# Kernel tuning notes

Hardware: AMD Instinct MI355X
Metric: run time of the kernel (lower is better)

Reference implementation:

```python
import jax, jax.numpy as jnp
import numpy as np

B, T, D, H = 32, 512, 512, 8
DH = D // H  # 64


def _pos_enc(t, d):
    # pos / 10000^(2i/d) for ALL i, then sin on even cols, cos on odd cols, scaled by sqrt(d)
    pos = np.arange(t, dtype=np.float64)[:, None]
    i = np.arange(d, dtype=np.float64)[None, :]
    ang = pos / np.power(10000.0, 2.0 * i / d)
    pe = np.empty((t, d), dtype=np.float64)
    pe[:, 0::2] = np.sin(ang[:, 0::2])
    pe[:, 1::2] = np.cos(ang[:, 1::2])
    return jnp.asarray(pe * np.sqrt(float(d)), dtype=jnp.float32)


def setup_inputs() -> dict:
    key = jax.random.key(0)
    ks = jax.random.split(key, 9)
    return {
        "queries": jax.random.normal(ks[0], (B, T, D), dtype=jnp.float32),
        "keys": jax.random.normal(ks[1], (B, T, D), dtype=jnp.float32),
        "query_masks": jax.random.randint(ks[2], (B,), 0, T, dtype=jnp.int32),
        "key_masks": jax.random.randint(ks[3], (B,), 0, T, dtype=jnp.int32),
        "W_Q": jax.random.normal(ks[4], (D, D), dtype=jnp.float32) * 0.05,
        "W_K": jax.random.normal(ks[5], (D, D), dtype=jnp.float32) * 0.05,
        "W_V": jax.random.normal(ks[6], (D, D), dtype=jnp.float32) * 0.05,
        "fw1": jax.random.normal(ks[7], (D, 4 * D), dtype=jnp.float32) * 0.05,
        "fw2": jax.random.normal(ks[8], (4 * D, D), dtype=jnp.float32) * 0.05,
    }


def reference(queries, keys, query_masks, key_masks, W_Q, W_K, W_V, fw1, fw2):
    pe = _pos_enc(T, D)  # [T, D]
    # Source bug kept: queries = posenc(queries); keys = posenc(queries)  -> keys input unused
    q1 = queries + pe[None]          # [B,T,D]
    k1 = q1 + pe[None]               # pos-encoded twice
    Q = q1 @ W_Q                     # [B,T,D]
    Kp = k1 @ W_K                    # [B,T,D]
    V = Kp @ W_V                     # source bug kept: values from projected keys
    # split heads (head-major fold in the original concat(split) idiom)
    Qh = Q.reshape(B, T, H, DH).transpose(2, 0, 1, 3)   # [H,B,T,dh]
    Kh = Kp.reshape(B, T, H, DH).transpose(2, 0, 1, 3)
    Vh = V.reshape(B, T, H, DH).transpose(2, 0, 1, 3)
    scores = jnp.einsum('hbqd,hbkd->hbqk', Qh, Kh) / jnp.sqrt(jnp.float32(DH))
    # source subtracts max over the QUERY axis (axis=1 of [H*B,T,T]) = axis 2 here
    scores = scores - scores.max(axis=2, keepdims=True)
    attn = jax.nn.softmax(scores, axis=-1)
    qmask = (jnp.arange(T)[None, :] < query_masks[:, None]).astype(jnp.float32)  # [B,T]
    attn = attn * qmask[None, :, :, None]
    out = jnp.einsum('hbqk,hbkd->hbqd', attn, Vh)       # [H,B,T,dh]
    result = out.transpose(1, 2, 0, 3).reshape(B, T, D) + q1  # residual with pos-encoded queries
    hidden = jax.nn.relu(result @ fw1)                  # [B,T,4D]
    result = result + hidden @ fw2                      # residual; no layer norm (use_layer_norm=False)
    return result
```

## Files before the change

kernel.cpp:

```cpp
#include <hip/hip_runtime.h>
#include <cstdint>
#include <cstddef>

typedef __bf16 bf16x8 __attribute__((ext_vector_type(8)));
typedef float f32x4 __attribute__((ext_vector_type(4)));
using u16 = unsigned short;
using u32 = unsigned int;

__device__ __forceinline__ u16 f2b(float f) {
  u32 u = __float_as_uint(f);
  u32 r = u + 0x7FFFu + ((u >> 16) & 1u);
  return (u16)(r >> 16);
}
__device__ __forceinline__ float b2f(u16 h) { return __uint_as_float((u32)h << 16); }

__device__ __forceinline__ void gload16(const void* g, void* l) {
  __builtin_amdgcn_global_load_lds((const __attribute__((address_space(1))) void*)g,
                                   (__attribute__((address_space(3))) void*)l, 16, 0, 0);
}

__device__ __forceinline__ u32 mapf(float f) {
  u32 u = __float_as_uint(f);
  return (u & 0x80000000u) ? ~u : (u | 0x80000000u);
}
__device__ __forceinline__ float unmapf(u32 k) {
  u32 u = (k & 0x80000000u) ? (k ^ 0x80000000u) : ~k;
  return __uint_as_float(u);
}
__device__ __forceinline__ u32 cvtpk(float lo, float hi) {
  u32 r;
  asm("v_cvt_pk_bf16_f32 %0, %1, %2" : "=v"(r) : "v"(lo), "v"(hi));
  return r;
}

#define MFMA __builtin_amdgcn_mfma_f32_16x16x32_bf16

__global__ void pe_kernel(float* __restrict__ pe) {
  int i = blockIdx.x * 256 + threadIdx.x;
  if (i >= 512 * 512) return;
  int t = i >> 9, d = i & 511;
  double ang = (double)t * exp((double)d * (-2.0 / 512.0) * log(10000.0));
  double v = (d & 1) ? cos(ang) : sin(ang);
  pe[i] = (float)(v * 22.627416997969522);
}

__global__ __launch_bounds__(256) void wprep_kernel(
    const float* __restrict__ WQ, const float* __restrict__ WK, const float* __restrict__ WV,
    const float* __restrict__ f1, const float* __restrict__ f2, u16* __restrict__ WQth,
    u16* __restrict__ WQtl, u16* __restrict__ WKth, u16* __restrict__ WKtl,
    u16* __restrict__ WVt, u16* __restrict__ f1t, u16* __restrict__ f2t,
    u16* __restrict__ WKb) {
  __shared__ float tile[64][65];
  const int bid = blockIdx.x, t = threadIdx.x;
  if (bid >= 704) {
    int i4 = (bid - 704) * 256 + t;
    float4 v = *(const float4*)&WK[i4 * 4];
    ushort4 o = {f2b(v.x), f2b(v.y), f2b(v.z), f2b(v.w)};
    *(ushort4*)&WKb[i4 * 4] = o;
    return;
  }
  const float* in;
  int R, C, bx, by;
  u16 *oh, *ol;
  bool split;
  if (bid < 64) {
    in = WQ; R = 512; C = 512; oh = WQth; ol = WQtl; split = true; bx = bid % 8; by = bid / 8;
  } else if (bid < 128) {
    int l = bid - 64;
    in = WK; R = 512; C = 512; oh = WKth; ol = WKtl; split = true; bx = l % 8; by = l / 8;
  } else if (bid < 192) {
    int l = bid - 128;
    in = WV; R = 512; C = 512; oh = WVt; ol = nullptr; split = false; bx = l % 8; by = l / 8;
  } else if (bid < 448) {
    int l = bid - 192;
    in = f1; R = 512; C = 2048; oh = f1t; ol = nullptr; split = false; bx = l % 8; by = l / 8;
  } else {
    int l = bid - 448;
    in = f2; R = 2048; C = 512; oh = f2t; ol = nullptr; split = false; bx = l % 32; by = l / 32;
  }
  const long r0 = (long)bx * 64, c0 = (long)by * 64;
#pragma unroll
  for (int it = 0; it < 4; ++it) {
    int r = it * 16 + (t >> 4);
    int c = (t & 15) * 4;
    float4 v = *(const float4*)&in[(r0 + r) * C + c0 + c];
    tile[r][c] = v.x;
    tile[r][c + 1] = v.y;
    tile[r][c + 2] = v.z;
    tile[r][c + 3] = v.w;
  }
  __syncthreads();
#pragma unroll
  for (int it = 0; it < 4; ++it) {
    int oc = it * 16 + (t >> 4);
    int orr = (t & 15) * 4;
    ushort4 h4, l4;
    u16* hp = (u16*)&h4;
    u16* lp = (u16*)&l4;
#pragma unroll
    for (int j = 0; j < 4; ++j) {
      float v = tile[orr + j][oc];
      u16 h = f2b(v);
      hp[j] = h;
      if (split) lp[j] = f2b(v - b2f(h));
    }
    *(ushort4*)&oh[(c0 + oc) * R + r0 + orr] = h4;
    if (split) *(ushort4*)&ol[(c0 + oc) * R + r0 + orr] = l4;
  }
}

__global__ void prep_kernel(const float* __restrict__ q, const float* __restrict__ pe,
                            u16* __restrict__ q1h, u16* __restrict__ q1l,
                            u16* __restrict__ k1h, u16* __restrict__ k1l) {
  int i4 = blockIdx.x * 256 + threadIdx.x;
  if (i4 >= 2097152) return;
  int i = i4 * 4;
  int td = i & (262144 - 1);
  float4 qv = *(const float4*)&q[i];
  float4 pv = *(const float4*)&pe[td];
  float q1[4] = {qv.x + pv.x, qv.y + pv.y, qv.z + pv.z, qv.w + pv.w};
  float pp[4] = {pv.x, pv.y, pv.z, pv.w};
  ushort4 qh4, ql4, kh4, kl4;
  u16* qhp = (u16*)&qh4;
  u16* qlp = (u16*)&ql4;
  u16* khp = (u16*)&kh4;
  u16* klp = (u16*)&kl4;
#pragma unroll
  for (int j = 0; j < 4; ++j) {
    float k1 = q1[j] + pp[j];
    u16 h = f2b(q1[j]);
    qhp[j] = h;
    qlp[j] = f2b(q1[j] - b2f(h));
    h = f2b(k1);
    khp[j] = h;
    klp[j] = f2b(k1 - b2f(h));
  }
  *(ushort4*)&q1h[i] = qh4;
  *(ushort4*)&q1l[i] = ql4;
  *(ushort4*)&k1h[i] = kh4;
  *(ushort4*)&k1l[i] = kl4;
}

#define GM_BF16 0
#define GM_RELU 2
#define GM_ADDF32 3

template <int MODE>
__global__ __launch_bounds__(256, 3) void gemm_bt(const u16* __restrict__ A,
                                                  const u16* __restrict__ B, int M, int N, int K,
                                                  u16* __restrict__ outb, float* __restrict__ outf,
                                                  const float* __restrict__ res) {
  __shared__ u16 As[128 * 32];
  __shared__ u16 Bs[128 * 32];
  const int tid = threadIdx.x, lane = tid & 63, w = tid >> 6;
  const int wm = w >> 1, wn = w & 1;
  const long aBase = (long)blockIdx.x * 128;
  const long bBase = (long)blockIdx.y * 128;
  f32x4 acc[4][4] = {};
  const int nk = K >> 5;
  for (int kt = 0; kt < nk; ++kt) {
#pragma unroll
    for (int i = 0; i < 2; ++i) {
      const int c = w * 2 + i;
      const int off = c * 1024 + lane * 16;
      const int r = off >> 6, cb = off & 63;
      gload16((const char*)A + ((aBase + r) * (long)K + (long)kt * 32) * 2 + cb,
              (char*)As + c * 1024);
      gload16((const char*)B + ((bBase + r) * (long)K + (long)kt * 32) * 2 + cb,
              (char*)Bs + c * 1024);
    }
    __syncthreads();
    bf16x8 af[4], bfr[4];
#pragma unroll
    for (int x = 0; x < 4; ++x) {
      af[x] = *(const bf16x8*)&As[(wm * 64 + x * 16 + (lane & 15)) * 32 + (lane >> 4) * 8];
      bfr[x] = *(const bf16x8*)&Bs[(wn * 64 + x * 16 + (lane & 15)) * 32 + (lane >> 4) * 8];
    }
#pragma unroll
    for (int mf = 0; mf < 4; ++mf)
#pragma unroll
      for (int nf = 0; nf < 4; ++nf)
        acc[mf][nf] = MFMA(af[mf], bfr[nf], acc[mf][nf], 0, 0, 0);
    __syncthreads();
  }
#pragma unroll
  for (int mf = 0; mf < 4; ++mf)
#pragma unroll
    for (int nf = 0; nf < 4; ++nf) {
      const long row0 = aBase + wm * 64 + mf * 16 + (lane >> 4) * 4;
      const long col = bBase + wn * 64 + nf * 16 + (lane & 15);
#pragma unroll
      for (int j = 0; j < 4; ++j) {
        float v = acc[mf][nf][j];
        const long row = row0 + j;
        if constexpr (MODE == GM_BF16)
          outb[row * N + col] = f2b(v);
        else if constexpr (MODE == GM_RELU)
          outb[row * N + col] = f2b(v > 0.f ? v : 0.f);
        else
          outf[row * N + col] = res[row * N + col] + v;
      }
    }
}

__global__ __launch_bounds__(256, 3) void gemm_split(const u16* __restrict__ Ah,
                                                     const u16* __restrict__ Al,
                                                     const u16* __restrict__ Bh,
                                                     const u16* __restrict__ Bl, int M, int N,
                                                     int K, u16* __restrict__ Oh,
                                                     u16* __restrict__ Ol) {
  __shared__ u16 Ash[4096], Asl[4096], Bsh[4096], Bsl[4096];
  const int tid = threadIdx.x, lane = tid & 63, w = tid >> 6;
  const int wm = w >> 1, wn = w & 1;
  const long aBase = (long)blockIdx.x * 128;
  const long bBase = (long)blockIdx.y * 128;
  f32x4 acc[4][4] = {};
  const int nk = K >> 5;
  for (int kt = 0; kt < nk; ++kt) {
#pragma unroll
    for (int i = 0; i < 2; ++i) {
      const int c = w * 2 + i;
      const int off = c * 1024 + lane * 16;
      const int r = off >> 6, cb = off & 63;
      long ga = ((aBase + r) * (long)K + (long)kt * 32) * 2 + cb;
      long gb = ((bBase + r) * (long)K + (long)kt * 32) * 2 + cb;
      gload16((const char*)Ah + ga, (char*)Ash + c * 1024);
      gload16((const char*)Al + ga, (char*)Asl + c * 1024);
      gload16((const char*)Bh + gb, (char*)Bsh + c * 1024);
      gload16((const char*)Bl + gb, (char*)Bsl + c * 1024);
    }
    __syncthreads();
    bf16x8 ah[4], al[4], bh[4], bl[4];
#pragma unroll
    for (int x = 0; x < 4; ++x) {
      int ao = (wm * 64 + x * 16 + (lane & 15)) * 32 + (lane >> 4) * 8;
      int bo = (wn * 64 + x * 16 + (lane & 15)) * 32 + (lane >> 4) * 8;
      ah[x] = *(const bf16x8*)&Ash[ao];
      al[x] = *(const bf16x8*)&Asl[ao];
      bh[x] = *(const bf16x8*)&Bsh[bo];
      bl[x] = *(const bf16x8*)&Bsl[bo];
    }
#pragma unroll
    for (int mf = 0; mf < 4; ++mf)
#pragma unroll
      for (int nf = 0; nf < 4; ++nf) {
        acc[mf][nf] = MFMA(ah[mf], bh[nf], acc[mf][nf], 0, 0, 0);
        acc[mf][nf] = MFMA(ah[mf], bl[nf], acc[mf][nf], 0, 0, 0);
        acc[mf][nf] = MFMA(al[mf], bh[nf], acc[mf][nf], 0, 0, 0);
      }
    __syncthreads();
  }
#pragma unroll
  for (int mf = 0; mf < 4; ++mf)
#pragma unroll
    for (int nf = 0; nf < 4; ++nf) {
      const long row0 = aBase + wm * 64 + mf * 16 + (lane >> 4) * 4;
      const long col = bBase + wn * 64 + nf * 16 + (lane & 15);
#pragma unroll
      for (int j = 0; j < 4; ++j) {
        float v = acc[mf][nf][j];
        const long row = row0 + j;
        u16 h = f2b(v);
        Oh[row * N + col] = h;
        Ol[row * N + col] = f2b(v - b2f(h));
      }
    }
}

__global__ __launch_bounds__(512) void attn_fused(
    const u16* __restrict__ Qh, const u16* __restrict__ Ql, const u16* __restrict__ Kh,
    const u16* __restrict__ Kl, const u16* __restrict__ Vt, const int* __restrict__ qmask,
    const u16* __restrict__ r1h, const u16* __restrict__ r1l, float* __restrict__ resf,
    u16* __restrict__ resb) {
  extern __shared__ char smem[];
  u16* Khi = (u16*)smem;
  u16* Klo = (u16*)(smem + 65536);
  u32* mloc = (u32*)(smem + 131072);
  float* mksf = (float*)(smem + 131072);
  const int tid = threadIdx.x, lane = tid & 63, w = tid >> 6;
  const int qll = lane & 15, g = lane >> 4;
  const int hb = blockIdx.x, b = hb >> 3, h = hb & 7;
  const int qm = qmask[b];
  mloc[tid] = 0u;
  const int srccb = 16 * ((lane & 7) ^ ((lane >> 3) & 7));
#pragma unroll
  for (int c = 0; c < 8; ++c) {
    long gb = ((long)(b * 512 + c * 64 + w * 8 + (lane >> 3)) * 512 + h * 64) * 2 + srccb;
    gload16((const char*)Kh + gb, (char*)Khi + c * 8192 + w * 1024);
    gload16((const char*)Kl + gb, (char*)Klo + c * 8192 + w * 1024);
  }
  bf16x8 qfh[4][2], qfl[4][2];
#pragma unroll
  for (int s = 0; s < 4; ++s) {
    const long qr = (long)(b * 512 + w * 64 + s * 16 + qll) * 512 + h * 64 + g * 8;
    qfh[s][0] = *(const bf16x8*)&Qh[qr];
    qfh[s][1] = *(const bf16x8*)&Qh[qr + 32];
    qfl[s][0] = *(const bf16x8*)&Ql[qr];
    qfl[s][1] = *(const bf16x8*)&Ql[qr + 32];
  }
  __syncthreads();
  const int sw0 = 8 * (g ^ (qll & 7));
  const int sw1 = 8 * ((4 + g) ^ (qll & 7));
  for (int kc = 0; kc < 8; ++kc) {
    const int cb = kc * 4096;
    __builtin_amdgcn_s_setprio(1);
#pragma unroll
    for (int kt = 0; kt < 4; ++kt) {
      const int ko = cb + (kt * 16 + qll) * 64;
      bf16x8 kh0 = *(const bf16x8*)&Khi[ko + sw0];
      bf16x8 kl0 = *(const bf16x8*)&Klo[ko + sw0];
      bf16x8 kh1 = *(const bf16x8*)&Khi[ko + sw1];
      bf16x8 kl1 = *(const bf16x8*)&Klo[ko + sw1];
      float vmax = -3.0e38f;
#pragma unroll
      for (int s = 0; s < 4; ++s) {
        f32x4 acc = {0.f, 0.f, 0.f, 0.f};
        acc = MFMA(qfh[s][0], kh0, acc, 0, 0, 0);
        acc = MFMA(qfh[s][0], kl0, acc, 0, 0, 0);
        acc = MFMA(qfl[s][0], kh0, acc, 0, 0, 0);
        acc = MFMA(qfh[s][1], kh1, acc, 0, 0, 0);
        acc = MFMA(qfh[s][1], kl1, acc, 0, 0, 0);
        acc = MFMA(qfl[s][1], kh1, acc, 0, 0, 0);
        vmax = fmaxf(vmax, fmaxf(fmaxf(acc[0], acc[1]), fmaxf(acc[2], acc[3])));
      }
      vmax = fmaxf(vmax, __shfl_xor(vmax, 16));
      vmax = fmaxf(vmax, __shfl_xor(vmax, 32));
      if (lane < 16) atomicMax(&mloc[kc * 64 + kt * 16 + qll], mapf(vmax));
    }
    __builtin_amdgcn_s_setprio(0);
  }
  __syncthreads();
  float mv = 0.125f * unmapf(mloc[tid]);
  __syncthreads();
  mksf[tid] = mv;
  __syncthreads();
  const u16* vb = Vt + (long)(h * 64) * 16384 + b * 512;
  const int src0 = (g & 1) * 32 + qll;
  const int src1 = src0 + 16;
  const bool lowh = g < 2;
  f32x4 o[4][4] = {};
  float mr[4] = {-3.0e38f, -3.0e38f, -3.0e38f, -3.0e38f};
  float rsum[4] = {0.f, 0.f, 0.f, 0.f};
  for (int kc = 0; kc < 8; ++kc) {
    bf16x8 vf[2][4];
#pragma unroll
    for (int k2 = 0; k2 < 2; ++k2)
#pragma unroll
      for (int nf = 0; nf < 4; ++nf)
        vf[k2][nf] =
            *(const bf16x8*)&vb[(long)(nf * 16 + qll) * 16384 + (kc * 2 + k2) * 32 + g * 8];
    const int cb = kc * 4096;
    f32x4 s4[4][4] = {};
    __builtin_amdgcn_s_setprio(1);
#pragma unroll
    for (int kt = 0; kt < 4; ++kt) {
      const int ko = cb + (kt * 16 + qll) * 64;
      bf16x8 kh0 = *(const bf16x8*)&Khi[ko + sw0];
      bf16x8 kl0 = *(const bf16x8*)&Klo[ko + sw0];
      bf16x8 kh1 = *(const bf16x8*)&Khi[ko + sw1];
      bf16x8 kl1 = *(const bf16x8*)&Klo[ko + sw1];
#pragma unroll
      for (int s = 0; s < 4; ++s) {
        s4[s][kt] = MFMA(kh0, qfh[s][0], s4[s][kt], 0, 0, 0);
        s4[s][kt] = MFMA(kh0, qfl[s][0], s4[s][kt], 0, 0, 0);
        s4[s][kt] = MFMA(kl0, qfh[s][0], s4[s][kt], 0, 0, 0);
        s4[s][kt] = MFMA(kh1, qfh[s][1], s4[s][kt], 0, 0, 0);
        s4[s][kt] = MFMA(kh1, qfl[s][1], s4[s][kt], 0, 0, 0);
        s4[s][kt] = MFMA(kl1, qfh[s][1], s4[s][kt], 0, 0, 0);
      }
    }
    __builtin_amdgcn_s_setprio(0);
#pragma unroll
    for (int s = 0; s < 4; ++s) {
      float pm = mr[s];
#pragma unroll
      for (int kt = 0; kt < 4; ++kt) {
        f32x4 mrow = *(const f32x4*)&mksf[kc * 64 + kt * 16 + g * 4];
#pragma unroll
        for (int j = 0; j < 4; ++j) {
          float z = s4[s][kt][j] * 0.125f - mrow[j];
          s4[s][kt][j] = z;
          pm = fmaxf(pm, z);
        }
      }
      pm = fmaxf(pm, __shfl_xor(pm, 16));
      pm = fmaxf(pm, __shfl_xor(pm, 32));
      const float f = __expf(mr[s] - pm);
      mr[s] = pm;
      rsum[s] *= f;
#pragma unroll
      for (int nf = 0; nf < 4; ++nf) {
        o[s][nf][0] *= f;
        o[s][nf][1] *= f;
        o[s][nf][2] *= f;
        o[s][nf][3] *= f;
      }
      u32 pk0[4], pk1[4];
#pragma unroll
      for (int kt = 0; kt < 4; ++kt) {
        float p0 = __expf(s4[s][kt][0] - pm);
        float p1 = __expf(s4[s][kt][1] - pm);
        float p2 = __expf(s4[s][kt][2] - pm);
        float p3 = __expf(s4[s][kt][3] - pm);
        rsum[s] += (p0 + p1) + (p2 + p3);
        pk0[kt] = cvtpk(p0, p1);
        pk1[kt] = cvtpk(p2, p3);
      }
      __builtin_amdgcn_s_setprio(1);
#pragma unroll
      for (int k2 = 0; k2 < 2; ++k2) {
        const int fA = 2 * k2, fB = 2 * k2 + 1;
        u32 a00 = __shfl(pk0[fA], src0), b00 = __shfl(pk0[fB], src0);
        u32 a10 = __shfl(pk1[fA], src0), b10 = __shfl(pk1[fB], src0);
        u32 a01 = __shfl(pk0[fA], src1), b01 = __shfl(pk0[fB], src1);
        u32 a11 = __shfl(pk1[fA], src1), b11 = __shfl(pk1[fB], src1);
        union {
          u32 u[4];
          bf16x8 v;
        } pf;
        pf.u[0] = lowh ? a00 : b00;
        pf.u[1] = lowh ? a10 : b10;
        pf.u[2] = lowh ? a01 : b01;
        pf.u[3] = lowh ? a11 : b11;
#pragma unroll
        for (int nf = 0; nf < 4; ++nf) o[s][nf] = MFMA(vf[k2][nf], pf.v, o[s][nf], 0, 0, 0);
      }
      __builtin_amdgcn_s_setprio(0);
    }
  }
#pragma unroll
  for (int s = 0; s < 4; ++s) {
    rsum[s] += __shfl_xor(rsum[s], 16);
    rsum[s] += __shfl_xor(rsum[s], 32);
    const int qg = w * 64 + s * 16 + qll;
    const float sc = (qg < qm) ? (1.0f / rsum[s]) : 0.0f;
#pragma unroll
    for (int nf = 0; nf < 4; ++nf) {
      const int col = h * 64 + nf * 16 + g * 4;
      const long idx = (long)(b * 512 + qg) * 512 + col;
      ushort4 qh4 = *(const ushort4*)&r1h[idx];
      ushort4 ql4 = *(const ushort4*)&r1l[idx];
      float v0 = o[s][nf][0] * sc + b2f(qh4.x) + b2f(ql4.x);
      float v1 = o[s][nf][1] * sc + b2f(qh4.y) + b2f(ql4.y);
      float v2 = o[s][nf][2] * sc + b2f(qh4.z) + b2f(ql4.z);
      float v3 = o[s][nf][3] * sc + b2f(qh4.w) + b2f(ql4.w);
      *(float4*)&resf[idx] = make_float4(v0, v1, v2, v3);
      ushort4 rb = {f2b(v0), f2b(v1), f2b(v2), f2b(v3)};
      *(ushort4*)&resb[idx] = rb;
    }
  }
}

extern "C" void kernel_launch(void* const* d_in, const int* in_sizes, int n_in, void* d_out,
                              int out_size, void* d_ws, size_t ws_size, hipStream_t stream) {
  (void)in_sizes;
  (void)n_in;
  (void)out_size;
  (void)ws_size;
  const float* queries = (const float*)d_in[0];
  const int* qmask = (const int*)d_in[2];
  const float* WQ = (const float*)d_in[4];
  const float* WK = (const float*)d_in[5];
  const float* WV = (const float*)d_in[6];
  const float* f1 = (const float*)d_in[7];
  const float* f2 = (const float*)d_in[8];
  float* out = (float*)d_out;
  char* ws = (char*)d_ws;
  const size_t A = 16777216;
  u16* q1h = (u16*)(ws + 0 * A);
  u16* q1l = (u16*)(ws + 1 * A);
  u16* k1h = (u16*)(ws + 2 * A);
  u16* k1l = (u16*)(ws + 3 * A);
  u16* Qh = (u16*)(ws + 4 * A);
  u16* Ql = (u16*)(ws + 5 * A);
  u16* Kh = (u16*)(ws + 6 * A);
  u16* Kl = (u16*)(ws + 7 * A);
  u16* Vt = (u16*)(ws + 8 * A);
  u16* resb = (u16*)(ws + 9 * A);
  u16* hid = (u16*)(ws + 0 * A);
  float* pe = (float*)(ws + 10 * A);
  char* wbase = ws + 10 * A + 1572864;
  u16* WQth = (u16*)(wbase + 0 * 524288);
  u16* WQtl = (u16*)(wbase + 1 * 524288);
  u16* WKth = (u16*)(wbase + 2 * 524288);
  u16* WKtl = (u16*)(wbase + 3 * 524288);
  u16* WKb = (u16*)(wbase + 4 * 524288);
  u16* WVt_w = (u16*)(wbase + 5 * 524288);
  u16* WKVt = (u16*)(wbase + 6 * 524288);
  u16* f1t = (u16*)(wbase + 7 * 524288);
  u16* f2t = (u16*)(wbase + 7 * 524288 + 2097152);

  pe_kernel<<<1024, 256, 0, stream>>>(pe);
  wprep_kernel<<<960, 256, 0, stream>>>(WQ, WK, WV, f1, f2, WQth, WQtl, WKth, WKtl, WVt_w, f1t,
                                        f2t, WKb);
  prep_kernel<<<8192, 256, 0, stream>>>(queries, pe, q1h, q1l, k1h, k1l);
  gemm_bt<GM_BF16><<<dim3(4, 4), 256, 0, stream>>>(WVt_w, WKb, 512, 512, 512, WKVt, nullptr,
                                                   nullptr);
  gemm_split<<<dim3(128, 4), 256, 0, stream>>>(q1h, q1l, WQth, WQtl, 16384, 512, 512, Qh, Ql);
  gemm_split<<<dim3(128, 4), 256, 0, stream>>>(k1h, k1l, WKth, WKtl, 16384, 512, 512, Kh, Kl);
  gemm_bt<GM_BF16><<<dim3(4, 128), 256, 0, stream>>>(WKVt, k1h, 512, 16384, 512, Vt, nullptr,
                                                     nullptr);
  hipFuncSetAttribute((const void*)attn_fused, hipFuncAttributeMaxDynamicSharedMemorySize, 133120);
  attn_fused<<<256, 512, 133120, stream>>>(Qh, Ql, Kh, Kl, Vt, qmask, q1h, q1l, out, resb);
  gemm_bt<GM_RELU><<<dim3(128, 16), 256, 0, stream>>>(resb, f1t, 16384, 2048, 512, hid, nullptr,
                                                      nullptr);
  gemm_bt<GM_ADDF32><<<dim3(128, 4), 256, 0, stream>>>(hid, f2t, 16384, 512, 2048, nullptr, out,
                                                       out);
}
```

Baseline: 311.0 us.

## Fuse column-max pass into online-softmax loop, computing key-column max per chunk

Removes the separate first pass that recomputed all QK^T MFMAs just to find the per-key max over the query axis. The column max is now taken from the scores already computed in the main loop, reduced across lanes and combined across waves with LDS atomics plus a per-chunk barrier, then read back directly. It also pins the attention kernel to two waves per EU. This halves the QK^T MFMA work, at the cost of an extra __syncthreads per key chunk and extra shuffles and atomics.

```diff
diff --git a/kernel.cpp b/kernel.cpp
--- a/kernel.cpp
+++ b/kernel.cpp
@@ -267,7 +267,7 @@
     }
 }
 
-__global__ __launch_bounds__(512) void attn_fused(
+__global__ __launch_bounds__(512) __attribute__((amdgpu_waves_per_eu(2, 2))) void attn_fused(
     const u16* __restrict__ Qh, const u16* __restrict__ Ql, const u16* __restrict__ Kh,
     const u16* __restrict__ Kl, const u16* __restrict__ Vt, const int* __restrict__ qmask,
     const u16* __restrict__ r1h, const u16* __restrict__ r1l, float* __restrict__ resf,
@@ -276,7 +276,6 @@
   u16* Khi = (u16*)smem;
   u16* Klo = (u16*)(smem + 65536);
   u32* mloc = (u32*)(smem + 131072);
-  float* mksf = (float*)(smem + 131072);
   const int tid = threadIdx.x, lane = tid & 63, w = tid >> 6;
   const int qll = lane & 15, g = lane >> 4;
   const int hb = blockIdx.x, b = hb >> 3, h = hb & 7;
@@ -301,39 +300,6 @@
   __syncthreads();
   const int sw0 = 8 * (g ^ (qll & 7));
   const int sw1 = 8 * ((4 + g) ^ (qll & 7));
-  for (int kc = 0; kc < 8; ++kc) {
-    const int cb = kc * 4096;
-    __builtin_amdgcn_s_setprio(1);
-#pragma unroll
-    for (int kt = 0; kt < 4; ++kt) {
-      const int ko = cb + (kt * 16 + qll) * 64;
-      bf16x8 kh0 = *(const bf16x8*)&Khi[ko + sw0];
-      bf16x8 kl0 = *(const bf16x8*)&Klo[ko + sw0];
-      bf16x8 kh1 = *(const bf16x8*)&Khi[ko + sw1];
-      bf16x8 kl1 = *(const bf16x8*)&Klo[ko + sw1];
-      float vmax = -3.0e38f;
-#pragma unroll
-      for (int s = 0; s < 4; ++s) {
-        f32x4 acc = {0.f, 0.f, 0.f, 0.f};
-        acc = MFMA(qfh[s][0], kh0, acc, 0, 0, 0);
-        acc = MFMA(qfh[s][0], kl0, acc, 0, 0, 0);
-        acc = MFMA(qfl[s][0], kh0, acc, 0, 0, 0);
-        acc = MFMA(qfh[s][1], kh1, acc, 0, 0, 0);
-        acc = MFMA(qfh[s][1], kl1, acc, 0, 0, 0);
-        acc = MFMA(qfl[s][1], kh1, acc, 0, 0, 0);
-        vmax = fmaxf(vmax, fmaxf(fmaxf(acc[0], acc[1]), fmaxf(acc[2], acc[3])));
-      }
-      vmax = fmaxf(vmax, __shfl_xor(vmax, 16));
-      vmax = fmaxf(vmax, __shfl_xor(vmax, 32));
-      if (lane < 16) atomicMax(&mloc[kc * 64 + kt * 16 + qll], mapf(vmax));
-    }
-    __builtin_amdgcn_s_setprio(0);
-  }
-  __syncthreads();
-  float mv = 0.125f * unmapf(mloc[tid]);
-  __syncthreads();
-  mksf[tid] = mv;
-  __syncthreads();
   const u16* vb = Vt + (long)(h * 64) * 16384 + b * 512;
   const int src0 = (g & 1) * 32 + qll;
   const int src1 = src0 + 16;
@@ -342,13 +308,6 @@
   float mr[4] = {-3.0e38f, -3.0e38f, -3.0e38f, -3.0e38f};
   float rsum[4] = {0.f, 0.f, 0.f, 0.f};
   for (int kc = 0; kc < 8; ++kc) {
-    bf16x8 vf[2][4];
-#pragma unroll
-    for (int k2 = 0; k2 < 2; ++k2)
-#pragma unroll
-      for (int nf = 0; nf < 4; ++nf)
-        vf[k2][nf] =
-            *(const bf16x8*)&vb[(long)(nf * 16 + qll) * 16384 + (kc * 2 + k2) * 32 + g * 8];
     const int cb = kc * 4096;
     f32x4 s4[4][4] = {};
     __builtin_amdgcn_s_setprio(1);
@@ -371,17 +330,43 @@
     }
     __builtin_amdgcn_s_setprio(0);
 #pragma unroll
+    for (int kt = 0; kt < 4; ++kt)
+#pragma unroll
+      for (int j = 0; j < 4; ++j) {
+        float v = fmaxf(fmaxf(s4[0][kt][j], s4[1][kt][j]), fmaxf(s4[2][kt][j], s4[3][kt][j]));
+        v = fmaxf(v, __shfl_xor(v, 1));
+        v = fmaxf(v, __shfl_xor(v, 2));
+        v = fmaxf(v, __shfl_xor(v, 4));
+        v = fmaxf(v, __shfl_xor(v, 8));
+        if (qll == 0) atomicMax(&mloc[kc * 64 + kt * 16 + g * 4 + j], mapf(v));
+      }
+    __syncthreads();
+    bf16x8 vf[2][4];
+#pragma unroll
+    for (int k2 = 0; k2 < 2; ++k2)
+#pragma unroll
+      for (int nf = 0; nf < 4; ++nf)
+        vf[k2][nf] =
+            *(const bf16x8*)&vb[(long)(nf * 16 + qll) * 16384 + (kc * 2 + k2) * 32 + g * 8];
+#pragma unroll
     for (int s = 0; s < 4; ++s) {
       float pm = mr[s];
 #pragma unroll
       for (int kt = 0; kt < 4; ++kt) {
-        f32x4 mrow = *(const f32x4*)&mksf[kc * 64 + kt * 16 + g * 4];
-#pragma unroll
-        for (int j = 0; j < 4; ++j) {
-          float z = s4[s][kt][j] * 0.125f - mrow[j];
-          s4[s][kt][j] = z;
-          pm = fmaxf(pm, z);
-        }
+        uint4 mu = *(const uint4*)&mloc[kc * 64 + kt * 16 + g * 4];
+        float m0 = 0.125f * unmapf(mu.x);
+        float m1 = 0.125f * unmapf(mu.y);
+        float m2 = 0.125f * unmapf(mu.z);
+        float m3 = 0.125f * unmapf(mu.w);
+        float z0 = s4[s][kt][0] * 0.125f - m0;
+        float z1 = s4[s][kt][1] * 0.125f - m1;
+        float z2 = s4[s][kt][2] * 0.125f - m2;
+        float z3 = s4[s][kt][3] * 0.125f - m3;
+        s4[s][kt][0] = z0;
+        s4[s][kt][1] = z1;
+        s4[s][kt][2] = z2;
+        s4[s][kt][3] = z3;
+        pm = fmaxf(pm, fmaxf(fmaxf(z0, z1), fmaxf(z2, z3)));
       }
       pm = fmaxf(pm, __shfl_xor(pm, 16));
       pm = fmaxf(pm, __shfl_xor(pm, 32));
```

Measured after the change: 329.9 us. 1.06x slower.

## Fuse Q/K projections via linearity, fold pos-enc into prep, bf16 residual

Applied to the files above, without the earlier changes.

Since k1 = q1 + pe, the K projection is computed as q1@W_K plus a precomputed pe@W_K term, letting Q and K share one concatenated split-precision GEMM with N=1024 and dropping the k1 low-half buffer and second GEMM. The pos-encoding kernel is merged into the weight-prep launch, which also emits split bf16 pe for the small pe@W_K GEMM. The final FFN residual now reads the bf16 result buffer instead of re-reading fp32 output. This cuts launches and memory traffic, at the cost of some precision in the residual add and in how K is reconstructed.

```diff
diff --git a/kernel.cpp b/kernel.cpp
--- a/kernel.cpp
+++ b/kernel.cpp
@@ -35,23 +35,25 @@
 
 #define MFMA __builtin_amdgcn_mfma_f32_16x16x32_bf16
 
-__global__ void pe_kernel(float* __restrict__ pe) {
-  int i = blockIdx.x * 256 + threadIdx.x;
-  if (i >= 512 * 512) return;
-  int t = i >> 9, d = i & 511;
-  double ang = (double)t * exp((double)d * (-2.0 / 512.0) * log(10000.0));
-  double v = (d & 1) ? cos(ang) : sin(ang);
-  pe[i] = (float)(v * 22.627416997969522);
-}
-
 __global__ __launch_bounds__(256) void wprep_kernel(
     const float* __restrict__ WQ, const float* __restrict__ WK, const float* __restrict__ WV,
-    const float* __restrict__ f1, const float* __restrict__ f2, u16* __restrict__ WQth,
-    u16* __restrict__ WQtl, u16* __restrict__ WKth, u16* __restrict__ WKtl,
-    u16* __restrict__ WVt, u16* __restrict__ f1t, u16* __restrict__ f2t,
-    u16* __restrict__ WKb) {
-  __shared__ float tile[64][65];
+    const float* __restrict__ f1, const float* __restrict__ f2, u16* __restrict__ QKth,
+    u16* __restrict__ QKtl, u16* __restrict__ WVt, u16* __restrict__ f1t,
+    u16* __restrict__ f2t, u16* __restrict__ WKb, float* __restrict__ pe,
+    u16* __restrict__ peh, u16* __restrict__ pel) {
   const int bid = blockIdx.x, t = threadIdx.x;
+  if (bid >= 960) {
+    int i = (bid - 960) * 256 + t;
+    int tt = i >> 9, d = i & 511;
+    double ang = (double)tt * exp((double)d * (-2.0 / 512.0) * log(10000.0));
+    double v = (d & 1) ? cos(ang) : sin(ang);
+    float p = (float)(v * 22.627416997969522);
+    pe[i] = p;
+    u16 h = f2b(p);
+    peh[i] = h;
+    pel[i] = f2b(p - b2f(h));
+    return;
+  }
   if (bid >= 704) {
     int i4 = (bid - 704) * 256 + t;
     float4 v = *(const float4*)&WK[i4 * 4];
@@ -59,15 +61,17 @@
     *(ushort4*)&WKb[i4 * 4] = o;
     return;
   }
+  __shared__ float tile[64][65];
   const float* in;
   int R, C, bx, by;
   u16 *oh, *ol;
   bool split;
   if (bid < 64) {
-    in = WQ; R = 512; C = 512; oh = WQth; ol = WQtl; split = true; bx = bid % 8; by = bid / 8;
+    in = WQ; R = 512; C = 512; oh = QKth; ol = QKtl; split = true; bx = bid % 8; by = bid / 8;
   } else if (bid < 128) {
     int l = bid - 64;
-    in = WK; R = 512; C = 512; oh = WKth; ol = WKtl; split = true; bx = l % 8; by = l / 8;
+    in = WK; R = 512; C = 512; oh = QKth + 262144; ol = QKtl + 262144; split = true;
+    bx = l % 8; by = l / 8;
   } else if (bid < 192) {
     int l = bid - 128;
     in = WV; R = 512; C = 512; oh = WVt; ol = nullptr; split = false; bx = l % 8; by = l / 8;
@@ -111,7 +115,7 @@
 
 __global__ void prep_kernel(const float* __restrict__ q, const float* __restrict__ pe,
                             u16* __restrict__ q1h, u16* __restrict__ q1l,
-                            u16* __restrict__ k1h, u16* __restrict__ k1l) {
+                            u16* __restrict__ k1h) {
   int i4 = blockIdx.x * 256 + threadIdx.x;
   if (i4 >= 2097152) return;
   int i = i4 * 4;
@@ -120,36 +124,32 @@
   float4 pv = *(const float4*)&pe[td];
   float q1[4] = {qv.x + pv.x, qv.y + pv.y, qv.z + pv.z, qv.w + pv.w};
   float pp[4] = {pv.x, pv.y, pv.z, pv.w};
-  ushort4 qh4, ql4, kh4, kl4;
+  ushort4 qh4, ql4, kh4;
   u16* qhp = (u16*)&qh4;
   u16* qlp = (u16*)&ql4;
   u16* khp = (u16*)&kh4;
-  u16* klp = (u16*)&kl4;
 #pragma unroll
   for (int j = 0; j < 4; ++j) {
     float k1 = q1[j] + pp[j];
     u16 h = f2b(q1[j]);
     qhp[j] = h;
     qlp[j] = f2b(q1[j] - b2f(h));
-    h = f2b(k1);
-    khp[j] = h;
-    klp[j] = f2b(k1 - b2f(h));
+    khp[j] = f2b(k1);
   }
   *(ushort4*)&q1h[i] = qh4;
   *(ushort4*)&q1l[i] = ql4;
   *(ushort4*)&k1h[i] = kh4;
-  *(ushort4*)&k1l[i] = kl4;
 }
 
 #define GM_BF16 0
 #define GM_RELU 2
-#define GM_ADDF32 3
+#define GM_ADDB 4
 
 template <int MODE>
 __global__ __launch_bounds__(256, 3) void gemm_bt(const u16* __restrict__ A,
                                                   const u16* __restrict__ B, int M, int N, int K,
                                                   u16* __restrict__ outb, float* __restrict__ outf,
-                                                  const float* __restrict__ res) {
+                                                  const u16* __restrict__ res16) {
   __shared__ u16 As[128 * 32];
   __shared__ u16 Bs[128 * 32];
   const int tid = threadIdx.x, lane = tid & 63, w = tid >> 6;
@@ -198,17 +198,20 @@
         else if constexpr (MODE == GM_RELU)
           outb[row * N + col] = f2b(v > 0.f ? v : 0.f);
         else
-          outf[row * N + col] = res[row * N + col] + v;
-      }
-    }
-}
-
+          outf[row * N + col] = b2f(res16[row * N + col]) + v;
+      }
+    }
+}
+
+template <int OUT>
 __global__ __launch_bounds__(256, 3) void gemm_split(const u16* __restrict__ Ah,
                                                      const u16* __restrict__ Al,
                                                      const u16* __restrict__ Bh,
                                                      const u16* __restrict__ Bl, int M, int N,
                                                      int K, u16* __restrict__ Oh,
-                                                     u16* __restrict__ Ol) {
+                                                     u16* __restrict__ Ol,
+                                                     float* __restrict__ Of,
+                                                     const float* __restrict__ peadd) {
   __shared__ u16 Ash[4096], Asl[4096], Bsh[4096], Bsl[4096];
   const int tid = threadIdx.x, lane = tid & 63, w = tid >> 6;
   const int wm = w >> 1, wn = w & 1;
@@ -260,18 +263,24 @@
       for (int j = 0; j < 4; ++j) {
         float v = acc[mf][nf][j];
         const long row = row0 + j;
-        u16 h = f2b(v);
-        Oh[row * N + col] = h;
-        Ol[row * N + col] = f2b(v - b2f(h));
+        if constexpr (OUT == 1) {
+          if (col >= 512) v += peadd[(row & 511) * 512 + (col - 512)];
+        }
+        if constexpr (OUT == 2) {
+          Of[row * N + col] = v;
+        } else {
+          u16 h = f2b(v);
+          Oh[row * N + col] = h;
+          Ol[row * N + col] = f2b(v - b2f(h));
+        }
       }
     }
 }
 
 __global__ __launch_bounds__(512) void attn_fused(
-    const u16* __restrict__ Qh, const u16* __restrict__ Ql, const u16* __restrict__ Kh,
-    const u16* __restrict__ Kl, const u16* __restrict__ Vt, const int* __restrict__ qmask,
-    const u16* __restrict__ r1h, const u16* __restrict__ r1l, float* __restrict__ resf,
-    u16* __restrict__ resb) {
+    const u16* __restrict__ QKh, const u16* __restrict__ QKl, const u16* __restrict__ Vt,
+    const int* __restrict__ qmask, const u16* __restrict__ r1h, const u16* __restrict__ r1l,
+    float* __restrict__ resf, u16* __restrict__ resb) {
   extern __shared__ char smem[];
   u16* Khi = (u16*)smem;
   u16* Klo = (u16*)(smem + 65536);
@@ -285,18 +294,18 @@
   const int srccb = 16 * ((lane & 7) ^ ((lane >> 3) & 7));
 #pragma unroll
   for (int c = 0; c < 8; ++c) {
-    long gb = ((long)(b * 512 + c * 64 + w * 8 + (lane >> 3)) * 512 + h * 64) * 2 + srccb;
-    gload16((const char*)Kh + gb, (char*)Khi + c * 8192 + w * 1024);
-    gload16((const char*)Kl + gb, (char*)Klo + c * 8192 + w * 1024);
+    long gb = ((long)(b * 512 + c * 64 + w * 8 + (lane >> 3)) * 1024 + 512 + h * 64) * 2 + srccb;
+    gload16((const char*)QKh + gb, (char*)Khi + c * 8192 + w * 1024);
+    gload16((const char*)QKl + gb, (char*)Klo + c * 8192 + w * 1024);
   }
   bf16x8 qfh[4][2], qfl[4][2];
 #pragma unroll
   for (int s = 0; s < 4; ++s) {
-    const long qr = (long)(b * 512 + w * 64 + s * 16 + qll) * 512 + h * 64 + g * 8;
-    qfh[s][0] = *(const bf16x8*)&Qh[qr];
-    qfh[s][1] = *(const bf16x8*)&Qh[qr + 32];
-    qfl[s][0] = *(const bf16x8*)&Ql[qr];
-    qfl[s][1] = *(const bf16x8*)&Ql[qr + 32];
+    const long qr = (long)(b * 512 + w * 64 + s * 16 + qll) * 1024 + h * 64 + g * 8;
+    qfh[s][0] = *(const bf16x8*)&QKh[qr];
+    qfh[s][1] = *(const bf16x8*)&QKh[qr + 32];
+    qfl[s][0] = *(const bf16x8*)&QKl[qr];
+    qfl[s][1] = *(const bf16x8*)&QKl[qr + 32];
   }
   __syncthreads();
   const int sw0 = 8 * (g ^ (qll & 7));
@@ -470,40 +479,39 @@
   u16* q1h = (u16*)(ws + 0 * A);
   u16* q1l = (u16*)(ws + 1 * A);
   u16* k1h = (u16*)(ws + 2 * A);
-  u16* k1l = (u16*)(ws + 3 * A);
-  u16* Qh = (u16*)(ws + 4 * A);
-  u16* Ql = (u16*)(ws + 5 * A);
-  u16* Kh = (u16*)(ws + 6 * A);
-  u16* Kl = (u16*)(ws + 7 * A);
+  u16* QKh = (u16*)(ws + 4 * A);
+  u16* QKl = (u16*)(ws + 6 * A);
   u16* Vt = (u16*)(ws + 8 * A);
   u16* resb = (u16*)(ws + 9 * A);
   u16* hid = (u16*)(ws + 0 * A);
   float* pe = (float*)(ws + 10 * A);
   char* wbase = ws + 10 * A + 1572864;
-  u16* WQth = (u16*)(wbase + 0 * 524288);
-  u16* WQtl = (u16*)(wbase + 1 * 524288);
-  u16* WKth = (u16*)(wbase + 2 * 524288);
-  u16* WKtl = (u16*)(wbase + 3 * 524288);
-  u16* WKb = (u16*)(wbase + 4 * 524288);
-  u16* WVt_w = (u16*)(wbase + 5 * 524288);
-  u16* WKVt = (u16*)(wbase + 6 * 524288);
-  u16* f1t = (u16*)(wbase + 7 * 524288);
-  u16* f2t = (u16*)(wbase + 7 * 524288 + 2097152);
-
-  pe_kernel<<<1024, 256, 0, stream>>>(pe);
-  wprep_kernel<<<960, 256, 0, stream>>>(WQ, WK, WV, f1, f2, WQth, WQtl, WKth, WKtl, WVt_w, f1t,
-                                        f2t, WKb);
-  prep_kernel<<<8192, 256, 0, stream>>>(queries, pe, q1h, q1l, k1h, k1l);
+  u16* QKth = (u16*)(wbase);
+  u16* QKtl = (u16*)(wbase + 1048576);
+  u16* WKb = (u16*)(wbase + 2097152);
+  u16* WVt_w = (u16*)(wbase + 2621440);
+  u16* WKVt = (u16*)(wbase + 3145728);
+  u16* f1t = (u16*)(wbase + 3670016);
+  u16* f2t = (u16*)(wbase + 5767168);
+  u16* peh = (u16*)(wbase + 7864320);
+  u16* pel = (u16*)(wbase + 8388608);
+  float* PEK = (float*)(wbase + 8912896);
+
+  wprep_kernel<<<1984, 256, 0, stream>>>(WQ, WK, WV, f1, f2, QKth, QKtl, WVt_w, f1t, f2t, WKb,
+                                         pe, peh, pel);
+  prep_kernel<<<8192, 256, 0, stream>>>(queries, pe, q1h, q1l, k1h);
   gemm_bt<GM_BF16><<<dim3(4, 4), 256, 0, stream>>>(WVt_w, WKb, 512, 512, 512, WKVt, nullptr,
                                                    nullptr);
-  gemm_split<<<dim3(128, 4), 256, 0, stream>>>(q1h, q1l, WQth, WQtl, 16384, 512, 512, Qh, Ql);
-  gemm_split<<<dim3(128, 4), 256, 0, stream>>>(k1h, k1l, WKth, WKtl, 16384, 512, 512, Kh, Kl);
+  gemm_split<2><<<dim3(4, 4), 256, 0, stream>>>(peh, pel, QKth + 262144, QKtl + 262144, 512, 512,
+                                                512, nullptr, nullptr, PEK, nullptr);
+  gemm_split<1><<<dim3(128, 8), 256, 0, stream>>>(q1h, q1l, QKth, QKtl, 16384, 1024, 512, QKh,
+                                                  QKl, nullptr, PEK);
   gemm_bt<GM_BF16><<<dim3(4, 128), 256, 0, stream>>>(WKVt, k1h, 512, 16384, 512, Vt, nullptr,
                                                      nullptr);
   hipFuncSetAttribute((const void*)attn_fused, hipFuncAttributeMaxDynamicSharedMemorySize, 133120);
-  attn_fused<<<256, 512, 133120, stream>>>(Qh, Ql, Kh, Kl, Vt, qmask, q1h, q1l, out, resb);
+  attn_fused<<<256, 512, 133120, stream>>>(QKh, QKl, Vt, qmask, q1h, q1l, out, resb);
   gemm_bt<GM_RELU><<<dim3(128, 16), 256, 0, stream>>>(resb, f1t, 16384, 2048, 512, hid, nullptr,
                                                       nullptr);
-  gemm_bt<GM_ADDF32><<<dim3(128, 4), 256, 0, stream>>>(hid, f2t, 16384, 512, 2048, nullptr, out,
-                                                       out);
-}
+  gemm_bt<GM_ADDB><<<dim3(128, 4), 256, 0, stream>>>(hid, f2t, 16384, 512, 2048, nullptr, out,
+                                                     resb);
+}
```

New measurement: 333.1 us. 1.07x slower.
